# Optimization experiments

Hardware: AMD Instinct MI355X
Metric: run time of the kernel (lower is better)

Reference implementation:

```python
import jax, jax.numpy as jnp
import numpy as np

B = 16384
IN_DIM = 4096
H1, H2 = 128, 64
LATENT = 32
REPS = 3


def setup_inputs() -> dict:
    key = jax.random.key(0)
    ks = jax.random.split(key, 10)
    def lin(k, fan_in, fan_out):
        bound = 1.0 / np.sqrt(fan_in)
        kw, kb = jax.random.split(k)
        W = jax.random.uniform(kw, (fan_in, fan_out), jnp.float32, -bound, bound)
        b = jax.random.uniform(kb, (fan_out,), jnp.float32, -bound, bound)
        return W, b
    x = jax.random.normal(ks[0], (B, IN_DIM), jnp.float32)
    W1, b1 = lin(ks[1], IN_DIM, H1)
    W2, b2 = lin(ks[2], H1, H2)
    W3, b3 = lin(ks[3], H2, LATENT)
    qparams = jax.random.normal(ks[4], (REPS * 2 * LATENT,), jnp.float32)
    Wd, bd = lin(ks[5], LATENT, IN_DIM)
    return {"x": x, "W1": W1, "b1": b1, "W2": W2, "b2": b2,
            "W3": W3, "b3": b3, "qparams": qparams, "Wd": Wd, "bd": bd}


def _forward(x, W1, b1, W2, b2, W3, b3, qparams, Wd, bd):
    # Classical encoder (dropout inactive in eval mode)
    h = jax.nn.relu(x @ W1 + b1)          # [B, H1]
    h = jax.nn.relu(h @ W2 + b2)          # [B, H2]
    z = h @ W3 + b3                       # [B, LATENT]
    # Quantum decoder: circuit is AngleEmbedding (RX) of latent followed by
    # 2*REPS AngleEmbedding (RX) layers of params -- all RX on the same wire
    # commute and add, no entanglers => <Z_i> = cos(total angle on wire i).
    param_offset = qparams.reshape(2 * REPS, LATENT).sum(axis=0)  # [LATENT]
    q = jnp.cos(z + param_offset)         # [B, LATENT]
    # Classical decoder
    return q @ Wd + bd                    # [B, IN_DIM]


def reference(x, W1, b1, W2, b2, W3, b3, qparams, Wd, bd):
    return _forward(x, W1, b1, W2, b2, W3, b3, qparams, Wd, bd)
```

## Files before the change

### kernel.cpp

```cpp
#include <hip/hip_runtime.h>
#include <hip/hip_bf16.h>

#define B_SZ   16384
#define IN_DIM 4096
#define H1D    128
#define H2D    64
#define LAT    32

typedef _Float16 half8 __attribute__((ext_vector_type(8)));
typedef _Float16 half4 __attribute__((ext_vector_type(4)));
typedef float float4v __attribute__((ext_vector_type(4)));

#define WS_W2T  1048576
#define WS_W3T  1064960
#define WS_WDT  1069056
#define WS_B3O  1331200
#define WS_Q    1331328

__global__ __launch_bounds__(256) void prep_kernel(
    const float* __restrict__ W1, const float* __restrict__ W2,
    const float* __restrict__ W3, const float* __restrict__ Wd,
    const float* __restrict__ b3, const float* __restrict__ qp,
    _Float16* __restrict__ W1t, _Float16* __restrict__ W2t,
    _Float16* __restrict__ W3t, _Float16* __restrict__ Wdt,
    float* __restrict__ b3off)
{
    int t = blockIdx.x * 256 + threadIdx.x;
    if (t < IN_DIM * H1D) {
        int k = t >> 7, n = t & 127;
        W1t[n * IN_DIM + k] = (_Float16)W1[t];
    }
    if (t < LAT * IN_DIM) {
        int k = t >> 12, n = t & 4095;
        Wdt[n * LAT + k] = (_Float16)Wd[t];
    }
    if (t < H1D * H2D) {
        int k = t >> 6, n = t & 63;
        W2t[n * H1D + k] = (_Float16)W2[t];
    }
    if (t < H2D * LAT) {
        int k = t >> 5, n = t & 31;
        W3t[n * H2D + k] = (_Float16)W3[t];
    }
    if (t < LAT) {
        float s = b3[t];
        #pragma unroll
        for (int r = 0; r < 6; ++r) s += qp[r * LAT + t];
        b3off[t] = s;
    }
}

static __device__ __forceinline__ half8 cvt8(float4v v0, float4v v1) {
    half8 h;
    h[0] = (_Float16)v0[0]; h[1] = (_Float16)v0[1];
    h[2] = (_Float16)v0[2]; h[3] = (_Float16)v0[3];
    h[4] = (_Float16)v1[0]; h[5] = (_Float16)v1[1];
    h[6] = (_Float16)v1[2]; h[7] = (_Float16)v1[3];
    return h;
}

__global__ __launch_bounds__(256, 2) void encoder_kernel(
    const float* __restrict__ x,
    const _Float16* __restrict__ W1t, const _Float16* __restrict__ W2t,
    const _Float16* __restrict__ W3t,
    const float* __restrict__ b1, const float* __restrict__ b2,
    const float* __restrict__ b3off, _Float16* __restrict__ qout)
{
    __shared__ alignas(16) float part[4 * 32 * 132];
    __shared__ alignas(16) _Float16 h1s[32 * 136];
    _Float16* h2s = (_Float16*)part;

    const int tid  = threadIdx.x;
    const int lane = tid & 63;
    const int w    = tid >> 6;
    const int l15  = lane & 15;
    const int quad = lane >> 4;
    const int rb0  = blockIdx.x * 32;

    float4v acc[2][8];
    #pragma unroll
    for (int mg = 0; mg < 2; ++mg)
        #pragma unroll
        for (int ct = 0; ct < 8; ++ct)
            acc[mg][ct] = (float4v){0.f, 0.f, 0.f, 0.f};

    const float* xp0 = x + (size_t)(rb0 + l15) * IN_DIM + w * 1024 + quad * 8;
    const float* xp1 = xp0 + 16 * IN_DIM;
    const _Float16* wp[8];
    #pragma unroll
    for (int ct = 0; ct < 8; ++ct)
        wp[ct] = W1t + (size_t)(ct * 16 + l15) * IN_DIM + w * 1024 + quad * 8;

    #pragma unroll 2
    for (int kk = 0; kk < 32; ++kk) {
        const int ko = kk * 32;
        float4v x00 = *(const float4v*)(xp0 + ko);
        float4v x01 = *(const float4v*)(xp0 + ko + 4);
        float4v x10 = *(const float4v*)(xp1 + ko);
        float4v x11 = *(const float4v*)(xp1 + ko + 4);
        half8 a0 = cvt8(x00, x01);
        half8 a1 = cvt8(x10, x11);
        #pragma unroll
        for (int ct = 0; ct < 8; ++ct) {
            half8 b = *(const half8*)(wp[ct] + ko);
            acc[0][ct] = __builtin_amdgcn_mfma_f32_16x16x32_f16(a0, b, acc[0][ct], 0, 0, 0);
            acc[1][ct] = __builtin_amdgcn_mfma_f32_16x16x32_f16(a1, b, acc[1][ct], 0, 0, 0);
        }
    }

    {
        float* pw = part + w * (32 * 132);
        #pragma unroll
        for (int mg = 0; mg < 2; ++mg)
            #pragma unroll
            for (int ct = 0; ct < 8; ++ct)
                #pragma unroll
                for (int r = 0; r < 4; ++r)
                    pw[(mg * 16 + quad * 4 + r) * 132 + ct * 16 + l15] = acc[mg][ct][r];
    }
    __syncthreads();

    #pragma unroll
    for (int i = 0; i < 4; ++i) {
        int chunk = tid * 4 + i;
        int row = chunk >> 5;
        int c4  = chunk & 31;
        const float* p = part + row * 132 + c4 * 4;
        float4v s = *(const float4v*)(p)
                  + *(const float4v*)(p + 32 * 132)
                  + *(const float4v*)(p + 2 * 32 * 132)
                  + *(const float4v*)(p + 3 * 32 * 132);
        float4v bb = *(const float4v*)(b1 + c4 * 4);
        s = s + bb;
        half4 h;
        h[0] = (_Float16)(s[0] > 0.f ? s[0] : 0.f);
        h[1] = (_Float16)(s[1] > 0.f ? s[1] : 0.f);
        h[2] = (_Float16)(s[2] > 0.f ? s[2] : 0.f);
        h[3] = (_Float16)(s[3] > 0.f ? s[3] : 0.f);
        *(half4*)(h1s + row * 136 + c4 * 4) = h;
    }
    __syncthreads();

    {
        float bv2 = b2[w * 16 + l15];
        float4v a2[2] = {(float4v){bv2, bv2, bv2, bv2}, (float4v){bv2, bv2, bv2, bv2}};
        #pragma unroll
        for (int kk = 0; kk < 4; ++kk) {
            half8 b = *(const half8*)(W2t + (w * 16 + l15) * H1D + kk * 32 + quad * 8);
            half8 a0 = *(const half8*)(h1s + l15 * 136 + kk * 32 + quad * 8);
            half8 a1 = *(const half8*)(h1s + (16 + l15) * 136 + kk * 32 + quad * 8);
            a2[0] = __builtin_amdgcn_mfma_f32_16x16x32_f16(a0, b, a2[0], 0, 0, 0);
            a2[1] = __builtin_amdgcn_mfma_f32_16x16x32_f16(a1, b, a2[1], 0, 0, 0);
        }
        __syncthreads();
        #pragma unroll
        for (int mg = 0; mg < 2; ++mg)
            #pragma unroll
            for (int r = 0; r < 4; ++r) {
                float v = a2[mg][r];
                h2s[(mg * 16 + quad * 4 + r) * 72 + w * 16 + l15] = (_Float16)(v > 0.f ? v : 0.f);
            }
    }
    __syncthreads();

    {
        const int mg3 = w >> 1;
        const int ct3 = w & 1;
        const int c3  = ct3 * 16 + l15;
        float bv3 = b3off[c3];
        float4v a3 = (float4v){bv3, bv3, bv3, bv3};
        #pragma unroll
        for (int kk = 0; kk < 2; ++kk) {
            half8 a = *(const half8*)(h2s + (mg3 * 16 + l15) * 72 + kk * 32 + quad * 8);
            half8 b = *(const half8*)(W3t + c3 * H2D + kk * 32 + quad * 8);
            a3 = __builtin_amdgcn_mfma_f32_16x16x32_f16(a, b, a3, 0, 0, 0);
        }
        #pragma unroll
        for (int r = 0; r < 4; ++r) {
            int row = rb0 + mg3 * 16 + quad * 4 + r;
            qout[(size_t)row * LAT + c3] = (_Float16)cosf(a3[r]);
        }
    }
}

__global__ __launch_bounds__(256, 8) void decoder_kernel(
    const _Float16* __restrict__ qin, const _Float16* __restrict__ Wdt,
    const float* __restrict__ bd, float* __restrict__ out)
{
    const int tid  = threadIdx.x;
    const int lane = tid & 63;
    const int w    = tid >> 6;
    const int l15  = lane & 15;
    const int quad = lane >> 4;
    const int stripe   = blockIdx.x >> 2;
    const int colchunk = blockIdx.x & 3;
    const int rb    = stripe * 16;
    const int cbase = colchunk * 1024 + w * 256;

    half8 bq = *(const half8*)(qin + (size_t)(rb + l15) * LAT + quad * 8);

    const _Float16* wdp = Wdt + (size_t)(cbase + l15) * LAT + quad * 8;
    const float* bdp = bd + cbase + quad * 4;
    float* op = out + (size_t)(rb + l15) * IN_DIM + cbase + quad * 4;

    #pragma unroll 4
    for (int ct = 0; ct < 16; ++ct) {
        half8 aw = *(const half8*)(wdp + ct * 16 * LAT);
        float4v bias = *(const float4v*)(bdp + ct * 16);
        float4v o = __builtin_amdgcn_mfma_f32_16x16x32_f16(aw, bq, bias, 0, 0, 0);
        *(float4v*)(op + ct * 16) = o;
    }
}

extern "C" void kernel_launch(void* const* d_in, const int* in_sizes, int n_in,
                              void* d_out, int out_size, void* d_ws, size_t ws_size,
                              hipStream_t stream)
{
    const float* x  = (const float*)d_in[0];
    const float* W1 = (const float*)d_in[1];
    const float* b1 = (const float*)d_in[2];
    const float* W2 = (const float*)d_in[3];
    const float* b2 = (const float*)d_in[4];
    const float* W3 = (const float*)d_in[5];
    const float* b3 = (const float*)d_in[6];
    const float* qp = (const float*)d_in[7];
    const float* Wd = (const float*)d_in[8];
    const float* bd = (const float*)d_in[9];
    float* out = (float*)d_out;

    char* ws = (char*)d_ws;
    _Float16* W1t = (_Float16*)(ws);
    _Float16* W2t = (_Float16*)(ws + WS_W2T);
    _Float16* W3t = (_Float16*)(ws + WS_W3T);
    _Float16* Wdt = (_Float16*)(ws + WS_WDT);
    float*    b3o = (float*)(ws + WS_B3O);
    _Float16* qbuf= (_Float16*)(ws + WS_Q);

    prep_kernel<<<2048, 256, 0, stream>>>(W1, W2, W3, Wd, b3, qp, W1t, W2t, W3t, Wdt, b3o);
    encoder_kernel<<<512, 256, 0, stream>>>(x, W1t, W2t, W3t, b1, b2, b3o, qbuf);
    decoder_kernel<<<4096, 256, 0, stream>>>(qbuf, Wdt, bd, out);
}
```

Baseline: 527.7 us.

## Stage x tiles in LDS with double buffering and split encoder over output columns

The encoder now uses 512 threads per block, with each of 8 waves owning 16 output columns of the first layer over the full K, instead of splitting K across 4 waves and reducing partials in shared memory. Each block converts its x tile to fp16 and stages it cooperatively in a double-buffered LDS tile. The next chunk's global load overlaps the current chunk's MFMAs. This removes the cross-wave partial-sum reduction and the redundant per-wave x loads, but it adds a __syncthreads per K chunk and leaves only two MFMA accumulators per wave. That may expose more load latency.

```diff
diff --git a/kernel.cpp b/kernel.cpp
--- a/kernel.cpp
+++ b/kernel.cpp
@@ -59,16 +59,19 @@
     return h;
 }
 
-__global__ __launch_bounds__(256, 2) void encoder_kernel(
+#define XS_STRIDE 136
+#define XS_SZ     (32 * XS_STRIDE)
+
+__global__ __launch_bounds__(512, 2) void encoder_kernel(
     const float* __restrict__ x,
     const _Float16* __restrict__ W1t, const _Float16* __restrict__ W2t,
     const _Float16* __restrict__ W3t,
     const float* __restrict__ b1, const float* __restrict__ b2,
     const float* __restrict__ b3off, _Float16* __restrict__ qout)
 {
-    __shared__ alignas(16) float part[4 * 32 * 132];
+    __shared__ alignas(16) _Float16 xs[2 * XS_SZ];
     __shared__ alignas(16) _Float16 h1s[32 * 136];
-    _Float16* h2s = (_Float16*)part;
+    _Float16* h2s = xs;
 
     const int tid  = threadIdx.x;
     const int lane = tid & 63;
@@ -77,71 +80,61 @@
     const int quad = lane >> 4;
     const int rb0  = blockIdx.x * 32;
 
-    float4v acc[2][8];
-    #pragma unroll
-    for (int mg = 0; mg < 2; ++mg)
-        #pragma unroll
-        for (int ct = 0; ct < 8; ++ct)
-            acc[mg][ct] = (float4v){0.f, 0.f, 0.f, 0.f};
-
-    const float* xp0 = x + (size_t)(rb0 + l15) * IN_DIM + w * 1024 + quad * 8;
-    const float* xp1 = xp0 + 16 * IN_DIM;
-    const _Float16* wp[8];
-    #pragma unroll
-    for (int ct = 0; ct < 8; ++ct)
-        wp[ct] = W1t + (size_t)(ct * 16 + l15) * IN_DIM + w * 1024 + quad * 8;
-
-    #pragma unroll 2
-    for (int kk = 0; kk < 32; ++kk) {
-        const int ko = kk * 32;
-        float4v x00 = *(const float4v*)(xp0 + ko);
-        float4v x01 = *(const float4v*)(xp0 + ko + 4);
-        float4v x10 = *(const float4v*)(xp1 + ko);
-        float4v x11 = *(const float4v*)(xp1 + ko + 4);
-        half8 a0 = cvt8(x00, x01);
-        half8 a1 = cvt8(x10, x11);
-        #pragma unroll
-        for (int ct = 0; ct < 8; ++ct) {
-            half8 b = *(const half8*)(wp[ct] + ko);
-            acc[0][ct] = __builtin_amdgcn_mfma_f32_16x16x32_f16(a0, b, acc[0][ct], 0, 0, 0);
-            acc[1][ct] = __builtin_amdgcn_mfma_f32_16x16x32_f16(a1, b, acc[1][ct], 0, 0, 0);
-        }
-    }
+    const int srow = tid >> 4;
+    const int scol = (tid & 15) * 8;
+    const float* sx = x + (size_t)(rb0 + srow) * IN_DIM + scol;
+
+    float4v acc0 = (float4v){0.f, 0.f, 0.f, 0.f};
+    float4v acc1 = (float4v){0.f, 0.f, 0.f, 0.f};
+
+    const _Float16* wp = W1t + (size_t)(w * 16 + l15) * IN_DIM + quad * 8;
 
     {
-        float* pw = part + w * (32 * 132);
-        #pragma unroll
-        for (int mg = 0; mg < 2; ++mg)
-            #pragma unroll
-            for (int ct = 0; ct < 8; ++ct)
-                #pragma unroll
-                for (int r = 0; r < 4; ++r)
-                    pw[(mg * 16 + quad * 4 + r) * 132 + ct * 16 + l15] = acc[mg][ct][r];
+        float4v r0 = *(const float4v*)(sx);
+        float4v r1 = *(const float4v*)(sx + 4);
+        *(half8*)(xs + srow * XS_STRIDE + scol) = cvt8(r0, r1);
     }
     __syncthreads();
 
-    #pragma unroll
-    for (int i = 0; i < 4; ++i) {
-        int chunk = tid * 4 + i;
-        int row = chunk >> 5;
-        int c4  = chunk & 31;
-        const float* p = part + row * 132 + c4 * 4;
-        float4v s = *(const float4v*)(p)
-                  + *(const float4v*)(p + 32 * 132)
-                  + *(const float4v*)(p + 2 * 32 * 132)
-                  + *(const float4v*)(p + 3 * 32 * 132);
-        float4v bb = *(const float4v*)(b1 + c4 * 4);
-        s = s + bb;
-        half4 h;
-        h[0] = (_Float16)(s[0] > 0.f ? s[0] : 0.f);
-        h[1] = (_Float16)(s[1] > 0.f ? s[1] : 0.f);
-        h[2] = (_Float16)(s[2] > 0.f ? s[2] : 0.f);
-        h[3] = (_Float16)(s[3] > 0.f ? s[3] : 0.f);
-        *(half4*)(h1s + row * 136 + c4 * 4) = h;
+    for (int c = 0; c < 32; ++c) {
+        _Float16* cur = xs + (c & 1) * XS_SZ;
+        _Float16* nxt = xs + ((c + 1) & 1) * XS_SZ;
+
+        float4v r0, r1;
+        const bool have_next = (c + 1 < 32);
+        if (have_next) {
+            const float* s = sx + (c + 1) * 128;
+            r0 = *(const float4v*)(s);
+            r1 = *(const float4v*)(s + 4);
+        }
+
+        #pragma unroll
+        for (int ks = 0; ks < 4; ++ks) {
+            half8 a0 = *(const half8*)(cur + l15 * XS_STRIDE + ks * 32 + quad * 8);
+            half8 a1 = *(const half8*)(cur + (16 + l15) * XS_STRIDE + ks * 32 + quad * 8);
+            half8 b  = *(const half8*)(wp + c * 128 + ks * 32);
+            acc0 = __builtin_amdgcn_mfma_f32_16x16x32_f16(a0, b, acc0, 0, 0, 0);
+            acc1 = __builtin_amdgcn_mfma_f32_16x16x32_f16(a1, b, acc1, 0, 0, 0);
+        }
+
+        if (have_next)
+            *(half8*)(nxt + srow * XS_STRIDE + scol) = cvt8(r0, r1);
+        __syncthreads();
+    }
+
+    {
+        float bv1 = b1[w * 16 + l15];
+        #pragma unroll
+        for (int r = 0; r < 4; ++r) {
+            float v0 = acc0[r] + bv1;
+            float v1 = acc1[r] + bv1;
+            h1s[(quad * 4 + r) * 136 + w * 16 + l15]      = (_Float16)(v0 > 0.f ? v0 : 0.f);
+            h1s[(16 + quad * 4 + r) * 136 + w * 16 + l15] = (_Float16)(v1 > 0.f ? v1 : 0.f);
+        }
     }
     __syncthreads();
 
-    {
+    if (w < 4) {
         float bv2 = b2[w * 16 + l15];
         float4v a2[2] = {(float4v){bv2, bv2, bv2, bv2}, (float4v){bv2, bv2, bv2, bv2}};
         #pragma unroll
@@ -152,7 +145,6 @@
             a2[0] = __builtin_amdgcn_mfma_f32_16x16x32_f16(a0, b, a2[0], 0, 0, 0);
             a2[1] = __builtin_amdgcn_mfma_f32_16x16x32_f16(a1, b, a2[1], 0, 0, 0);
         }
-        __syncthreads();
         #pragma unroll
         for (int mg = 0; mg < 2; ++mg)
             #pragma unroll
@@ -163,7 +155,7 @@
     }
     __syncthreads();
 
-    {
+    if (w < 4) {
         const int mg3 = w >> 1;
         const int ct3 = w & 1;
         const int c3  = ct3 * 16 + l15;
@@ -237,6 +229,6 @@
     _Float16* qbuf= (_Float16*)(ws + WS_Q);
 
     prep_kernel<<<2048, 256, 0, stream>>>(W1, W2, W3, Wd, b3, qp, W1t, W2t, W3t, Wdt, b3o);
-    encoder_kernel<<<512, 256, 0, stream>>>(x, W1t, W2t, W3t, b1, b2, b3o, qbuf);
+    encoder_kernel<<<512, 512, 0, stream>>>(x, W1t, W2t, W3t, b1, b2, b3o, qbuf);
     decoder_kernel<<<4096, 256, 0, stream>>>(qbuf, Wdt, bd, out);
 }
```

Result: faster. 491.7 us (-6.8%).
